# Kernel tuning notes

Measured on AMD Instinct MI355X. Metric: run time of the kernel, lower is better.

Reference implementation:

```python
import jax, jax.numpy as jnp
import numpy as np

THRESHOLD = 0.6


def _conv(x, w, b, pad):
    # x: [B,C,H,W], w: [O,I,kh,kw]
    y = jax.lax.conv_general_dilated(
        x, w, window_strides=(1, 1), padding=[(pad, pad), (pad, pad)],
        dimension_numbers=("NCHW", "OIHW", "NCHW"))
    return y + b[None, :, None, None]


def _avg_pool3(x):
    # F.avg_pool2d(x, 3, stride=1, padding=1) with count_include_pad=True -> divide by 9
    s = jax.lax.reduce_window(x, 0.0, jax.lax.add, (1, 1, 3, 3), (1, 1, 1, 1),
                              [(0, 0), (0, 0), (1, 1), (1, 1)])
    return s / 9.0


def _head(feat, w1, b1, w2, b2, w3, b3):
    h = jax.nn.relu(_conv(feat, w1, b1, 1))
    h = jax.nn.relu(_conv(h, w2, b2, 1))
    return _conv(h, w3, b3, 0)


def _normalize_atten(a):
    # per-sample min-max over spatial dims
    B = a.shape[0]
    flat = a.reshape(B, -1)
    mn = flat.min(axis=1, keepdims=True)
    mx = flat.max(axis=1, keepdims=True)
    return ((flat - mn) / (mx - mn)).reshape(a.shape)


def setup_inputs() -> dict:
    key = jax.random.key(0)
    ks = jax.random.split(key, 16)
    B, C, H, W = 32, 512, 28, 28
    NC = 200
    x = jax.random.normal(ks[0], (B, C, H, W), dtype=jnp.float32)
    label = jax.random.randint(ks[1], (B, NC), 0, 2, dtype=jnp.int32)

    def conv_w(k, o, i, kh):
        std = 1.0 / np.sqrt(i * kh * kh)
        return jax.random.normal(k, (o, i, kh, kh), dtype=jnp.float32) * std

    inp = {"x": x, "label": label}
    # cls head
    inp["w1"] = conv_w(ks[2], 1024, 512, 3); inp["b1"] = jnp.zeros((1024,), jnp.float32)
    inp["w2"] = conv_w(ks[3], 1024, 1024, 3); inp["b2"] = jnp.zeros((1024,), jnp.float32)
    inp["w3"] = conv_w(ks[4], NC, 1024, 1); inp["b3"] = jnp.zeros((NC,), jnp.float32)
    # cls_erase head
    inp["we1"] = conv_w(ks[5], 1024, 512, 3); inp["be1"] = jnp.zeros((1024,), jnp.float32)
    inp["we2"] = conv_w(ks[6], 1024, 1024, 3); inp["be2"] = jnp.zeros((1024,), jnp.float32)
    inp["we3"] = conv_w(ks[7], NC, 1024, 1); inp["be3"] = jnp.zeros((NC,), jnp.float32)
    return inp


def reference(x, label, w1, b1, w2, b2, w3, b3, we1, be1, we2, be2, we3, be3):
    feat = _avg_pool3(x)                              # [B,512,H,W]
    out = _head(feat, w1, b1, w2, b2, w3, b3)         # [B,NC,H,W]
    logits_1 = out.mean(axis=(2, 3))                  # [B,NC]

    # get_atten_map (train mode): average of class maps for positive labels, vectorized
    lab = label.astype(out.dtype)                     # [B,NC] 0/1
    cnt = lab.sum(axis=1)                             # [B]
    atten = jnp.einsum("bc,bchw->bhw", lab, out) / jnp.maximum(cnt, 1.0)[:, None, None]
    atten = _normalize_atten(atten)                   # [B,H,W]

    # erase_feature_maps: zero where atten >= threshold
    mask = jnp.where(atten >= THRESHOLD, 0.0, 1.0)[:, None]  # [B,1,H,W]
    feat_erase = feat * mask

    out_erase = _head(feat_erase, we1, be1, we2, be2, we3, be3)
    logits_ers = out_erase.mean(axis=(2, 3))
    return jax.nn.sigmoid(logits_1), jax.nn.sigmoid(logits_ers)
```

## Files before the change

kernel.cpp:

```cpp
#include <hip/hip_runtime.h>
#include <hip/hip_bf16.h>
#include <stdint.h>


typedef __attribute__((ext_vector_type(8))) short short8;
typedef __attribute__((ext_vector_type(4))) float floatx4;

__device__ __forceinline__ unsigned short f2bf(float f) {
  union { float f; uint32_t u; } cv; cv.f = f;
  uint32_t u = cv.u;
  u += 0x7fffu + ((u >> 16) & 1u);
  return (unsigned short)(u >> 16);
}

__global__ void wprep3(const float* __restrict__ w, unsigned short* __restrict__ wt,
                       int O, int C) {
  int i = blockIdx.x * 256 + threadIdx.x;
  int total = 9 * O * C;
  if (i >= total) return;
  int p = i / (O * C);
  int r = i - p * O * C;
  int o = r / C;
  int c = r - o * C;
  wt[i] = f2bf(w[(size_t)(o * C + c) * 9 + p]);
}

__global__ void wprep1(const float* __restrict__ w, unsigned short* __restrict__ wt,
                       int O, int OP, int C) {
  int i = blockIdx.x * 256 + threadIdx.x;
  if (i >= OP * C) return;
  int o = i / C, c = i - o * C;
  wt[i] = (o < O) ? f2bf(w[(size_t)o * C + c]) : (unsigned short)0;
}

__global__ void avgpool_k(const float* __restrict__ x, unsigned short* __restrict__ fp) {
  const int C = 512;
  int b = blockIdx.x, r = blockIdx.y, cg = blockIdx.z;
  int t = threadIdx.x;
  __shared__ float xs[3 * 128 * 29];
  if (r == 0 || r == 29) {
    for (int i = t; i < 32 * 128; i += 256) {
      int c = i & 127, col = i >> 7;
      fp[((size_t)(b * 30 + r) * 32 + col) * C + cg * 128 + c] = 0;
    }
    return;
  }
  for (int i = t; i < 3 * 128 * 28; i += 256) {
    int dy = i / 3584;
    int rem = i - dy * 3584;
    int c = rem / 28, fx = rem - c * 28;
    int fy = r - 2 + dy;
    float v = (fy >= 0 && fy < 28)
                  ? x[((size_t)(b * 512 + cg * 128 + c) * 28 + fy) * 28 + fx]
                  : 0.f;
    xs[(dy * 128 + c) * 29 + fx] = v;
  }
  __syncthreads();
  for (int i = t; i < 32 * 128; i += 256) {
    int c = i & 127, col = i >> 7;
    float v = 0.f;
    if (col >= 1 && col <= 28) {
      int fx0 = col - 1;
#pragma unroll
      for (int dy = 0; dy < 3; ++dy)
#pragma unroll
        for (int dx = 0; dx < 3; ++dx) {
          int fx = fx0 - 1 + dx;
          if (fx >= 0 && fx < 28) v += xs[(dy * 128 + c) * 29 + fx];
        }
      v *= (1.f / 9.f);
    }
    fp[((size_t)(b * 30 + r) * 32 + col) * C + cg * 128 + c] = f2bf(v);
  }
}

__global__ void zero_borders(unsigned short* __restrict__ h1,
                             unsigned short* __restrict__ h2, int Mch) {
  int i = blockIdx.x * 256 + threadIdx.x;
  int vch = Mch >> 3;
  int perbuf = 32 * 176 * vch;
  if (i >= 2 * perbuf) return;
  unsigned short* h = (i < perbuf) ? h1 : h2;
  int j = (i < perbuf) ? i : i - perbuf;
  int cv = j % vch;
  int rr = j / vch;
  int bidx = rr / 176, e = rr - bidx * 176;
  int row, col;
  if (e < 32)      { row = 0;  col = e; }
  else if (e < 64) { row = 29; col = e - 32; }
  else {
    int q = e - 64;
    row = 1 + (q >> 2);
    int k = q & 3;
    col = (k == 0) ? 0 : 28 + k;
  }
  size_t addr = ((size_t)(bidx * 30 + row) * 32 + col) * Mch + cv * 8;
  *(uint4*)&h[addr] = (uint4){0u, 0u, 0u, 0u};
}

template <int P, int RELU, int PADOUT, int XBITS>
__global__ __launch_bounds__(256, 2)
void conv_mfma(const unsigned short* __restrict__ fin,
               const unsigned short* __restrict__ wt,
               const float* __restrict__ bias,
               void* __restrict__ outp, int C, int M, int OB) {
  const int tid = threadIdx.x;
  const int lane = tid & 63;
  const int wave = tid >> 6;
  const int hB = wave & 1;
  const int wo = wave >> 1;
  const int ln = lane & 15;
  const int kq = lane >> 4;

  const int id = blockIdx.x;
  const int xo = id & ((1 << XBITS) - 1);
  const int s  = id >> XBITS;
  const int yo = s % 7;
  const int bz = s / 7;

  const int o0 = xo * 128 + wo * 64;
  const int wO0 = xo * 128;
  const int yo0 = yo * 4;
  const int b0 = bz * 2;
  const int bb = b0 + hB;

  __shared__ unsigned short ldsA[2 * 1536 * 8];
  __shared__ unsigned short ldsW[2 * 512 * 8];

  int baserc[7];
#pragma unroll
  for (int mi = 0; mi < 7; ++mi) {
    int n = mi * 16 + ln;
    int y = n / 28, x = n - y * 28;
    baserc[mi] = y * 32 + x;
  }
  const int wbase = wo * 2048 + ln * 32 + ((kq ^ (ln & 3)) << 3);

  floatx4 acc[7][4];
#pragma unroll
  for (int mi = 0; mi < 7; ++mi)
#pragma unroll
    for (int ni = 0; ni < 4; ++ni)
      acc[mi][ni] = (floatx4){0.f, 0.f, 0.f, 0.f};

  const size_t fin_base0 = (size_t)(b0 * 30 + yo0) * 32 * C;
  const size_t fin_base1 = (size_t)((b0 + 1) * 30 + yo0) * 32 * C;

  const int rA = tid >> 2;
  const int cgA = (tid & 3) ^ (rA & 3);

  auto stageA = [&](int ck, int buf) {
#pragma unroll
    for (int it = 0; it < 6; ++it) {
      int wb = (it >= 3) ? 1 : 0;
      int it3 = it - wb * 3;
      int rc = it3 * 64 + rA;
      size_t goff = (wb ? fin_base1 : fin_base0) + (size_t)rc * C + ck + cgA * 8;
      unsigned short* lp = &ldsA[(unsigned)(buf * 1536 + wb * 768 + it3 * 256 + wave * 64) << 3];
      __builtin_amdgcn_global_load_lds((const uint32_t*)(fin + goff), (uint32_t*)lp,
                                       16, 0, 0);
    }
  };
  auto stageW = [&](int p, int ck, int buf) {
#pragma unroll
    for (int it = 0; it < 2; ++it) {
      int row = it * 64 + rA;
      size_t goff = (size_t)(p * M + wO0 + row) * C + ck + cgA * 8;
      unsigned short* lp = &ldsW[(unsigned)(buf * 512 + it * 256 + wave * 64) << 3];
      __builtin_amdgcn_global_load_lds((const uint32_t*)(wt + goff), (uint32_t*)lp,
                                       16, 0, 0);
    }
  };

  stageA(0, 0);
  stageW(0, 0, 0);

  int cur = 0;
  int wpar = 0;
  for (int ck = 0; ck < C; ck += 32) {
    const bool last = (ck + 32 >= C);
#pragma unroll
    for (int p = 0; p < P; ++p) {
      const bool fin_phase = last && (p == P - 1);

      __builtin_amdgcn_s_barrier();
      __builtin_amdgcn_sched_barrier(0);

      if (!fin_phase)
        stageW((p == P - 1) ? 0 : p + 1, (p == P - 1) ? ck + 32 : ck, wpar ^ 1);
      if (p == 0 && !last) stageA(ck + 32, cur ^ 1);

      if (fin_phase)               asm volatile("s_waitcnt vmcnt(0)" ::: "memory");
      else if (p <= 1 && !last)    asm volatile("s_waitcnt vmcnt(8)" ::: "memory");
      else                         asm volatile("s_waitcnt vmcnt(2)" ::: "memory");
      __builtin_amdgcn_sched_barrier(0);

      __builtin_amdgcn_s_barrier();
      __builtin_amdgcn_sched_barrier(0);
      asm volatile("" ::: "memory");

      const unsigned short* wrd = &ldsW[(unsigned)wpar << 12];
      const unsigned short* ard = &ldsA[cur ? 12288 : 0];
      int dy, dx;
      if (P == 1) { dy = 1; dx = 1; } else { dy = p / 3; dx = p - dy * 3; }
      short8 wf[4];
#pragma unroll
      for (int ni = 0; ni < 4; ++ni)
        wf[ni] = *(const short8*)(const void*)&wrd[wbase + ni * 512];
      short8 af[7];
#pragma unroll
      for (int mi = 0; mi < 7; ++mi) {
        int rc = baserc[mi] + dy * 32 + dx;
        int u = hB * 768 + (rc << 2) + (kq ^ (rc & 3));
        af[mi] = *(const short8*)(const void*)&ard[(unsigned)u << 3];
      }
      __builtin_amdgcn_s_setprio(1);
#pragma unroll
      for (int mi = 0; mi < 7; ++mi)
#pragma unroll
        for (int ni = 0; ni < 4; ++ni)
          acc[mi][ni] = __builtin_amdgcn_mfma_f32_16x16x32_bf16(af[mi], wf[ni],
                                                                acc[mi][ni], 0, 0, 0);
      __builtin_amdgcn_s_setprio(0);
      wpar ^= 1;
    }
    cur ^= 1;
  }

  float bia[4];
#pragma unroll
  for (int ni = 0; ni < 4; ++ni) {
    int o = o0 + ni * 16 + ln;
    bia[ni] = (o < OB) ? bias[o] : 0.f;
  }
#pragma unroll
  for (int mi = 0; mi < 7; ++mi) {
#pragma unroll
    for (int j = 0; j < 4; ++j) {
      int n = mi * 16 + kq * 4 + j;
      int y = n / 28, x = n - y * 28;
#pragma unroll
      for (int ni = 0; ni < 4; ++ni) {
        int o = o0 + ni * 16 + ln;
        float v = acc[mi][ni][j] + bia[ni];
        if (RELU) v = fmaxf(v, 0.f);
        if (PADOUT) {
          size_t addr = ((size_t)(bb * 30 + yo0 + y + 1) * 32 + (x + 1)) * M + o;
          ((unsigned short*)outp)[addr] = f2bf(v);
        } else {
          size_t addr = ((size_t)bb * 784 + (yo0 + y) * 28 + x) * M + o;
          ((float*)outp)[addr] = v;
        }
      }
    }
  }
}

template <int DO_ATTEN>
__global__ void logits_atten(const float* __restrict__ ob, const int* __restrict__ label,
                             float* __restrict__ outp, float* __restrict__ mask) {
  int b = blockIdx.x, t = threadIdx.x;
  const float* base = ob + (size_t)b * 784 * 256;
  float s = 0.f;
#pragma unroll 16
  for (int n = 0; n < 784; ++n) s += base[(size_t)n * 256 + t];
  if (t < 200) outp[b * 200 + t] = 1.f / (1.f + expf(-s * (1.f / 784.f)));

  if (DO_ATTEN) {
    __shared__ float labf[256];
    __shared__ float red[16];
    labf[t] = (t < 200) ? (float)label[b * 200 + t] : 0.f;
    __syncthreads();
    float att[4];
    float mn = 1e30f, mx = -1e30f;
#pragma unroll
    for (int i = 0; i < 4; ++i) {
      int n = t + i * 256;
      float a = 0.f;
      if (n < 784) {
        const float* rowp = base + (size_t)n * 256;
#pragma unroll 8
        for (int c = 0; c < 200; ++c) a += labf[c] * rowp[c];
        mn = fminf(mn, a);
        mx = fmaxf(mx, a);
      }
      att[i] = a;
    }
    for (int off = 32; off; off >>= 1) {
      mn = fminf(mn, __shfl_down(mn, off, 64));
      mx = fmaxf(mx, __shfl_down(mx, off, 64));
    }
    if ((t & 63) == 0) { red[(t >> 6) * 2] = mn; red[(t >> 6) * 2 + 1] = mx; }
    __syncthreads();
    if (t == 0) {
      float a = red[0], c = red[1];
      for (int wv = 1; wv < 4; ++wv) {
        a = fminf(a, red[wv * 2]);
        c = fmaxf(c, red[wv * 2 + 1]);
      }
      red[0] = a; red[1] = c;
    }
    __syncthreads();
    float gmn = red[0];
    float inv = 1.f / (red[1] - gmn);
#pragma unroll
    for (int i = 0; i < 4; ++i) {
      int n = t + i * 256;
      if (n < 784)
        mask[b * 784 + n] = ((att[i] - gmn) * inv >= 0.6f) ? 0.f : 1.f;
    }
  }
}

__global__ void erase_k(unsigned short* __restrict__ fp, const float* __restrict__ mask) {
  int i = blockIdx.x * 256 + threadIdx.x;
  if (i >= 32 * 28 * 28 * 512) return;
  int c = i & 511;
  int r2 = i >> 9;
  int xcol = r2 % 28;
  int r3 = r2 / 28;
  int y = r3 % 28;
  int b = r3 / 28;
  if (mask[b * 784 + y * 28 + xcol] == 0.f)
    fp[((size_t)(b * 30 + y + 1) * 32 + (xcol + 1)) * 512 + c] = 0;
}

extern "C" void kernel_launch(void* const* d_in, const int* in_sizes, int n_in,
                              void* d_out, int out_size, void* d_ws, size_t ws_size,
                              hipStream_t stream) {
  const float* x   = (const float*)d_in[0];
  const int* label = (const int*)d_in[1];
  const float* w1  = (const float*)d_in[2];
  const float* b1  = (const float*)d_in[3];
  const float* w2  = (const float*)d_in[4];
  const float* b2  = (const float*)d_in[5];
  const float* w3  = (const float*)d_in[6];
  const float* b3  = (const float*)d_in[7];
  const float* we1 = (const float*)d_in[8];
  const float* be1 = (const float*)d_in[9];
  const float* we2 = (const float*)d_in[10];
  const float* be2 = (const float*)d_in[11];
  const float* we3 = (const float*)d_in[12];
  const float* be3 = (const float*)d_in[13];
  float* outv = (float*)d_out;

  char* wp = (char*)d_ws;
  unsigned short* featp = (unsigned short*)wp; wp += 31457280;
  unsigned short* h1p   = (unsigned short*)wp; wp += 62914560;
  unsigned short* h2p   = (unsigned short*)wp; wp += 62914560;
  unsigned short* Wt1   = (unsigned short*)wp; wp += 9437184;
  unsigned short* Wt2   = (unsigned short*)wp; wp += 18874368;
  unsigned short* Wt3   = (unsigned short*)wp; wp += 524288;
  float* outbuf         = (float*)wp;          wp += 25690112;
  float* maskb          = (float*)wp;          wp += 100352;

  zero_borders<<<5632, 256, 0, stream>>>(h1p, h2p, 1024);
  avgpool_k<<<dim3(32, 30, 4), 256, 0, stream>>>(x, featp);
  wprep3<<<(9 * 1024 * 512 + 255) / 256, 256, 0, stream>>>(w1, Wt1, 1024, 512);
  wprep3<<<(9 * 1024 * 1024 + 255) / 256, 256, 0, stream>>>(w2, Wt2, 1024, 1024);
  wprep1<<<(256 * 1024 + 255) / 256, 256, 0, stream>>>(w3, Wt3, 200, 256, 1024);

  conv_mfma<9, 1, 1, 3><<<896, 256, 0, stream>>>(featp, Wt1, b1, h1p, 512, 1024, 1024);
  conv_mfma<9, 1, 1, 3><<<896, 256, 0, stream>>>(h1p, Wt2, b2, h2p, 1024, 1024, 1024);
  conv_mfma<1, 0, 0, 1><<<224, 256, 0, stream>>>(h2p, Wt3, b3, outbuf, 1024, 256, 200);
  logits_atten<1><<<32, 256, 0, stream>>>(outbuf, label, outv, maskb);

  erase_k<<<(32 * 28 * 28 * 512 + 255) / 256, 256, 0, stream>>>(featp, maskb);
  wprep3<<<(9 * 1024 * 512 + 255) / 256, 256, 0, stream>>>(we1, Wt1, 1024, 512);
  wprep3<<<(9 * 1024 * 1024 + 255) / 256, 256, 0, stream>>>(we2, Wt2, 1024, 1024);
  wprep1<<<(256 * 1024 + 255) / 256, 256, 0, stream>>>(we3, Wt3, 200, 256, 1024);
  conv_mfma<9, 1, 1, 3><<<896, 256, 0, stream>>>(featp, Wt1, be1, h1p, 512, 1024, 1024);
  conv_mfma<9, 1, 1, 3><<<896, 256, 0, stream>>>(h1p, Wt2, be2, h2p, 1024, 1024, 1024);
  conv_mfma<1, 0, 0, 1><<<224, 256, 0, stream>>>(h2p, Wt3, be3, outbuf, 1024, 256, 200);
  logits_atten<0><<<32, 256, 0, stream>>>(outbuf, nullptr, outv + 6400, nullptr);
}
```

Baseline: 3.872 ms.

## Deepen weight prefetch to a 4-slot ring and remap block order

The weight tile staging in the MFMA conv kernel moves from double buffering to a 4-slot ring. Weights are prefetched three taps ahead, and the vmcnt wait counts are adjusted to match. The block index mapping also changes so consecutive blocks share the same output-channel slice rather than the same spatial tile, which alters L2 reuse patterns. This adds LDS usage, which could limit occupancy, and makes the wait-count logic more intricate.

Measured after the change: 3.634 ms. 1.07x faster.

```diff
diff --git a/kernel.cpp b/kernel.cpp
--- a/kernel.cpp
+++ b/kernel.cpp
@@ -98,7 +98,7 @@
   *(uint4*)&h[addr] = (uint4){0u, 0u, 0u, 0u};
 }
 
-template <int P, int RELU, int PADOUT, int XBITS>
+template <int P, int RELU, int PADOUT>
 __global__ __launch_bounds__(256, 2)
 void conv_mfma(const unsigned short* __restrict__ fin,
                const unsigned short* __restrict__ wt,
@@ -113,8 +113,8 @@
   const int kq = lane >> 4;
 
   const int id = blockIdx.x;
-  const int xo = id & ((1 << XBITS) - 1);
-  const int s  = id >> XBITS;
+  const int xo = id / 112;
+  const int s  = id - xo * 112;
   const int yo = s % 7;
   const int bz = s / 7;
 
@@ -125,7 +125,7 @@
   const int bb = b0 + hB;
 
   __shared__ unsigned short ldsA[2 * 1536 * 8];
-  __shared__ unsigned short ldsW[2 * 512 * 8];
+  __shared__ unsigned short ldsW[4 * 512 * 8];
 
   int baserc[7];
 #pragma unroll
@@ -161,12 +161,12 @@
                                        16, 0, 0);
     }
   };
-  auto stageW = [&](int p, int ck, int buf) {
+  auto stageW = [&](int p, int ck, int q) {
 #pragma unroll
     for (int it = 0; it < 2; ++it) {
       int row = it * 64 + rA;
       size_t goff = (size_t)(p * M + wO0 + row) * C + ck + cgA * 8;
-      unsigned short* lp = &ldsW[(unsigned)(buf * 512 + it * 256 + wave * 64) << 3];
+      unsigned short* lp = &ldsW[(unsigned)(q * 512 + it * 256 + wave * 64) << 3];
       __builtin_amdgcn_global_load_lds((const uint32_t*)(wt + goff), (uint32_t*)lp,
                                        16, 0, 0);
     }
@@ -174,9 +174,10 @@
 
   stageA(0, 0);
   stageW(0, 0, 0);
+  if (P == 9) { stageW(1, 0, 1); stageW(2, 0, 2); }
 
   int cur = 0;
-  int wpar = 0;
+  int rq0 = 0;
   for (int ck = 0; ck < C; ck += 32) {
     const bool last = (ck + 32 >= C);
 #pragma unroll
@@ -186,20 +187,32 @@
       __builtin_amdgcn_s_barrier();
       __builtin_amdgcn_sched_barrier(0);
 
-      if (!fin_phase)
-        stageW((p == P - 1) ? 0 : p + 1, (p == P - 1) ? ck + 32 : ck, wpar ^ 1);
+      if (P == 9) {
+        if (!(last && p >= 6))
+          stageW(p < 6 ? p + 3 : p - 6, p < 6 ? ck : ck + 32, (rq0 + p + 3) & 3);
+      } else {
+        if (!last) stageW(0, ck + 32, (rq0 + p + 1) & 3);
+      }
       if (p == 0 && !last) stageA(ck + 32, cur ^ 1);
 
-      if (fin_phase)               asm volatile("s_waitcnt vmcnt(0)" ::: "memory");
-      else if (p <= 1 && !last)    asm volatile("s_waitcnt vmcnt(8)" ::: "memory");
-      else                         asm volatile("s_waitcnt vmcnt(2)" ::: "memory");
+      if (P == 9) {
+        if (fin_phase)           asm volatile("s_waitcnt vmcnt(0)" ::: "memory");
+        else if (last && p == 6) asm volatile("s_waitcnt vmcnt(4)" ::: "memory");
+        else if (last && p == 7) asm volatile("s_waitcnt vmcnt(2)" ::: "memory");
+        else if (last)           asm volatile("s_waitcnt vmcnt(6)" ::: "memory");
+        else if (p <= 3)         asm volatile("s_waitcnt vmcnt(12)" ::: "memory");
+        else                     asm volatile("s_waitcnt vmcnt(6)" ::: "memory");
+      } else {
+        if (last)                asm volatile("s_waitcnt vmcnt(0)" ::: "memory");
+        else                     asm volatile("s_waitcnt vmcnt(8)" ::: "memory");
+      }
       __builtin_amdgcn_sched_barrier(0);
 
       __builtin_amdgcn_s_barrier();
       __builtin_amdgcn_sched_barrier(0);
       asm volatile("" ::: "memory");
 
-      const unsigned short* wrd = &ldsW[(unsigned)wpar << 12];
+      const unsigned short* wrd = &ldsW[(unsigned)(((rq0 + p) & 3) << 12)];
       const unsigned short* ard = &ldsA[cur ? 12288 : 0];
       int dy, dx;
       if (P == 1) { dy = 1; dx = 1; } else { dy = p / 3; dx = p - dy * 3; }
@@ -222,8 +235,8 @@
           acc[mi][ni] = __builtin_amdgcn_mfma_f32_16x16x32_bf16(af[mi], wf[ni],
                                                                 acc[mi][ni], 0, 0, 0);
       __builtin_amdgcn_s_setprio(0);
-      wpar ^= 1;
-    }
+    }
+    rq0 = (rq0 + P) & 3;
     cur ^= 1;
   }
 
@@ -360,17 +373,17 @@
   wprep3<<<(9 * 1024 * 1024 + 255) / 256, 256, 0, stream>>>(w2, Wt2, 1024, 1024);
   wprep1<<<(256 * 1024 + 255) / 256, 256, 0, stream>>>(w3, Wt3, 200, 256, 1024);
 
-  conv_mfma<9, 1, 1, 3><<<896, 256, 0, stream>>>(featp, Wt1, b1, h1p, 512, 1024, 1024);
-  conv_mfma<9, 1, 1, 3><<<896, 256, 0, stream>>>(h1p, Wt2, b2, h2p, 1024, 1024, 1024);
-  conv_mfma<1, 0, 0, 1><<<224, 256, 0, stream>>>(h2p, Wt3, b3, outbuf, 1024, 256, 200);
+  conv_mfma<9, 1, 1><<<896, 256, 0, stream>>>(featp, Wt1, b1, h1p, 512, 1024, 1024);
+  conv_mfma<9, 1, 1><<<896, 256, 0, stream>>>(h1p, Wt2, b2, h2p, 1024, 1024, 1024);
+  conv_mfma<1, 0, 0><<<224, 256, 0, stream>>>(h2p, Wt3, b3, outbuf, 1024, 256, 200);
   logits_atten<1><<<32, 256, 0, stream>>>(outbuf, label, outv, maskb);
 
   erase_k<<<(32 * 28 * 28 * 512 + 255) / 256, 256, 0, stream>>>(featp, maskb);
   wprep3<<<(9 * 1024 * 512 + 255) / 256, 256, 0, stream>>>(we1, Wt1, 1024, 512);
   wprep3<<<(9 * 1024 * 1024 + 255) / 256, 256, 0, stream>>>(we2, Wt2, 1024, 1024);
   wprep1<<<(256 * 1024 + 255) / 256, 256, 0, stream>>>(we3, Wt3, 200, 256, 1024);
-  conv_mfma<9, 1, 1, 3><<<896, 256, 0, stream>>>(featp, Wt1, be1, h1p, 512, 1024, 1024);
-  conv_mfma<9, 1, 1, 3><<<896, 256, 0, stream>>>(h1p, Wt2, be2, h2p, 1024, 1024, 1024);
-  conv_mfma<1, 0, 0, 1><<<224, 256, 0, stream>>>(h2p, Wt3, be3, outbuf, 1024, 256, 200);
+  conv_mfma<9, 1, 1><<<896, 256, 0, stream>>>(featp, Wt1, be1, h1p, 512, 1024, 1024);
+  conv_mfma<9, 1, 1><<<896, 256, 0, stream>>>(h1p, Wt2, be2, h2p, 1024, 1024, 1024);
+  conv_mfma<1, 0, 0><<<224, 256, 0, stream>>>(h2p, Wt3, be3, outbuf, 1024, 256, 200);
   logits_atten<0><<<32, 256, 0, stream>>>(outbuf, nullptr, outv + 6400, nullptr);
 }
```
